# Kernel optimization log

Hardware: AMD Instinct MI355X
Metric: run time of the kernel (lower is better)

The kernel has to match this reference:

```python
import jax, jax.numpy as jnp
import numpy as np
import math

B, T, C, H = 2, 2048, 1024, 16
D = C // H  # head dim = 64

def setup_inputs() -> dict:
    key = jax.random.key(0)
    ks = jax.random.split(key, 9)
    s = 0.02
    return {
        "x": jax.random.normal(ks[0], (B, T, C), dtype=jnp.float32),
        "Wq": jax.random.normal(ks[1], (C, C), dtype=jnp.float32) * s,
        "bq": jax.random.normal(ks[2], (C,), dtype=jnp.float32) * s,
        "Wk": jax.random.normal(ks[3], (C, C), dtype=jnp.float32) * s,
        "bk": jax.random.normal(ks[4], (C,), dtype=jnp.float32) * s,
        "Wv": jax.random.normal(ks[5], (C, C), dtype=jnp.float32) * s,
        "bv": jax.random.normal(ks[6], (C,), dtype=jnp.float32) * s,
        "Wo": jax.random.normal(ks[7], (C, C), dtype=jnp.float32) * s,
        "bo": jax.random.normal(ks[8], (C,), dtype=jnp.float32) * s,
    }

def reference(x, Wq, bq, Wk, bk, Wv, bv, Wo, bo):
    # x: [B, T, C]; torch Linear is y = x @ W.T + b
    Bv_, Tv_, Cv_ = x.shape
    q = (x @ Wq.T + bq).reshape(Bv_, Tv_, H, D)
    k = (x @ Wk.T + bk).reshape(Bv_, Tv_, H, D)
    v = (x @ Wv.T + bv).reshape(Bv_, Tv_, H, D)
    scale = 1.0 / math.sqrt(D)
    # [B, H, Tq, Tk] attention scores
    att = jnp.einsum("bqhd,bkhd->bhqk", q, k) * scale
    causal = jnp.tril(jnp.ones((Tv_, Tv_), dtype=bool))  # [T, T]
    att = jnp.where(causal[None, None, :, :], att, -jnp.inf)
    att = jax.nn.softmax(att, axis=-1)
    y = jnp.einsum("bhqk,bkhd->bqhd", att, v).reshape(Bv_, Tv_, Cv_)
    return y @ Wo.T + bo
```

## Files before the change

kernel.cpp:

```cpp
#include <hip/hip_runtime.h>
#include <hip/hip_bf16.h>
#include <cstdint>
#include <cstddef>

typedef __attribute__((ext_vector_type(8))) short short8;
typedef __attribute__((ext_vector_type(4))) float f32x4;
typedef unsigned int u32;
typedef __attribute__((ext_vector_type(4))) u32 u32x4;

#define MFMA(a,b,c) __builtin_amdgcn_mfma_f32_16x16x32_bf16(a,b,c,0,0,0)

__device__ __forceinline__ void gload_lds16(const void* gptr, void* lptr) {
  __builtin_amdgcn_global_load_lds((const __attribute__((address_space(1))) u32*)gptr,
                                   (__attribute__((address_space(3))) u32*)lptr, 16, 0, 0);
}

template<int N> __device__ __forceinline__ void vm_wait() {
  asm volatile("s_waitcnt vmcnt(%0)" :: "n"(N) : "memory");
}

__device__ __forceinline__ void barrier_sync() {
  asm volatile("" ::: "memory");
  __builtin_amdgcn_s_barrier();
  asm volatile("" ::: "memory");
  __builtin_amdgcn_sched_barrier(0);
}

__device__ __forceinline__ unsigned short f2bf(float f) {
  __hip_bfloat16 h = __float2bfloat16(f);
  return *reinterpret_cast<unsigned short*>(&h);
}

__device__ __forceinline__ short8 ldg8(const unsigned short* p) {
  return *reinterpret_cast<const short8*>(p);
}

__device__ __forceinline__ u32 cvt_pk_bf16(float lo, float hi) {
  u32 r;
  asm("v_cvt_pk_bf16_f32 %0, %1, %2" : "=v"(r) : "v"(lo), "v"(hi));
  return r;
}

__global__ __launch_bounds__(256) void cvt_all_kernel(
    const float* __restrict__ x,
    const float* __restrict__ w0, const float* __restrict__ w1,
    const float* __restrict__ w2, const float* __restrict__ w3,
    unsigned short* __restrict__ xb,
    unsigned short* __restrict__ o0, unsigned short* __restrict__ o1,
    unsigned short* __restrict__ o2, unsigned short* __restrict__ o3)
{
  int id = blockIdx.x * blockDim.x + threadIdx.x;
  const float* in;
  unsigned short* out;
  int idx;
  if (id < 1048576) {
    in = x; out = xb; idx = id;
  } else {
    int r = id - 1048576;
    int z = r >> 18;
    idx = r & 262143;
    in  = (z == 0) ? w0 : (z == 1) ? w1 : (z == 2) ? w2 : w3;
    out = (z == 0) ? o0 : (z == 1) ? o1 : (z == 2) ? o2 : o3;
  }
  float4 f = reinterpret_cast<const float4*>(in)[idx];
  ushort4 o;
  o.x = f2bf(f.x); o.y = f2bf(f.y); o.z = f2bf(f.z); o.w = f2bf(f.w);
  reinterpret_cast<ushort4*>(out)[idx] = o;
}

template<int BM, int BN, int WM, int WN, bool F32OUT>
__device__ __forceinline__ void gemm2_body(
    const unsigned short* __restrict__ A,
    const unsigned short* __restrict__ W,
    const float* __restrict__ bias,
    unsigned short* __restrict__ outb, float* __restrict__ outf,
    int ldo, float oscale, int m0)
{
  constexpr int K = 1024, BK = 32, NT = K / BK;
  constexpr int NTHR = WM * WN * 64;
  constexpr int FM = BM / (WM * 16);
  constexpr int FN = BN / (WN * 16);
  constexpr int NLA = BM * BK * 2 / (NTHR * 16);
  constexpr int NLB = BN * BK * 2 / (NTHR * 16);
  constexpr int NLD = NLA + NLB;

  __shared__ unsigned short As[2][BM * BK];
  __shared__ unsigned short Ws[2][BN * BK];

  const int tid = threadIdx.x;
  const int lane = tid & 63;
  const int wave = tid >> 6;
  const int wm = wave / WN, wn = wave % WN;
  const int wr = wm * FM * 16, wc = wn * FN * 16;
  const int lr = lane >> 4, lc = lane & 15;

  f32x4 acc[FM][FN] = {};

  const char* Ab = (const char*)(A + (size_t)m0 * K);
  const char* Wb = (const char*)W;

#define STAGE(buf, k0)                                                            \
  {                                                                               \
    _Pragma("unroll")                                                             \
    for (int i = 0; i < NLA; ++i) {                                               \
      int L = (i * NTHR + tid) * 16;                                              \
      int row = L >> 6;                                                           \
      int col = L & 63;                                                           \
      gload_lds16(Ab + (size_t)row * 2048 + (k0) * 2 + col, (char*)&As[buf][0] + L); \
    }                                                                             \
    _Pragma("unroll")                                                             \
    for (int i = 0; i < NLB; ++i) {                                               \
      int L = (i * NTHR + tid) * 16;                                              \
      int row = L >> 6;                                                           \
      int col = L & 63;                                                           \
      gload_lds16(Wb + (size_t)row * 2048 + (k0) * 2 + col, (char*)&Ws[buf][0] + L); \
    }                                                                             \
  }

#define COMPUTE(buf)                                                              \
  {                                                                               \
    short8 af[FM], bf[FN];                                                        \
    _Pragma("unroll")                                                             \
    for (int m = 0; m < FM; ++m) {                                                \
      int row = wr + m * 16 + lc;                                                 \
      af[m] = *reinterpret_cast<const short8*>(                                   \
          (const char*)&As[buf][0] + row * 64 + lr * 16);                         \
    }                                                                             \
    _Pragma("unroll")                                                             \
    for (int n = 0; n < FN; ++n) {                                                \
      int row = wc + n * 16 + lc;                                                 \
      bf[n] = *reinterpret_cast<const short8*>(                                   \
          (const char*)&Ws[buf][0] + row * 64 + lr * 16);                         \
    }                                                                             \
    __builtin_amdgcn_s_setprio(1);                                                \
    _Pragma("unroll")                                                             \
    for (int m = 0; m < FM; ++m)                                                  \
      _Pragma("unroll")                                                           \
      for (int n = 0; n < FN; ++n)                                                \
        acc[m][n] = MFMA(af[m], bf[n], acc[m][n]);                                \
    __builtin_amdgcn_s_setprio(0);                                                \
  }

  STAGE(0, 0)
  STAGE(1, BK)
  int cur = 0;
#pragma unroll 1
  for (int kt = 0; kt < NT - 2; ++kt) {
    vm_wait<NLD>();
    barrier_sync();
    COMPUTE(cur)
    barrier_sync();
    STAGE(cur, (kt + 2) * BK)
    cur ^= 1;
  }
  vm_wait<NLD>();
  barrier_sync();
  COMPUTE(cur)
  cur ^= 1;
  vm_wait<0>();
  barrier_sync();
  COMPUTE(cur)

#undef STAGE
#undef COMPUTE

#pragma unroll
  for (int m = 0; m < FM; ++m)
#pragma unroll
    for (int n = 0; n < FN; ++n)
#pragma unroll
      for (int r = 0; r < 4; ++r) {
        int row = m0 + wr + m * 16 + lr * 4 + r;
        int col = wc + n * 16 + lc;
        float v = (acc[m][n][r] + bias[col]) * oscale;
        if (F32OUT) outf[(size_t)row * ldo + col] = v;
        else        outb[(size_t)row * ldo + col] = f2bf(v);
      }
}

__global__ __launch_bounds__(256, 3) void gemm_qkv5(
    const unsigned short* __restrict__ xb,
    const unsigned short* __restrict__ Wqb, const unsigned short* __restrict__ Wkb,
    const unsigned short* __restrict__ Wvb,
    const float* __restrict__ bq, const float* __restrict__ bk, const float* __restrict__ bv,
    unsigned short* __restrict__ Q, unsigned short* __restrict__ Ko, unsigned short* __restrict__ V)
{
  const int i = blockIdx.x;
  const int sw = (i & 7) * 96 + (i >> 3);
  const int z  = sw >> 8;
  const int rr = sw & 255;
  const int m0 = (rr >> 3) * 128;
  const int nr = (rr & 7) * 128;
  const unsigned short* W = ((z == 0) ? Wqb : (z == 1) ? Wkb : Wvb) + (size_t)nr * 1024;
  const float* bias = ((z == 0) ? bq : (z == 1) ? bk : bv) + nr;
  unsigned short* out = ((z == 0) ? Q : (z == 1) ? Ko : V) + nr;
  const float oscale = (z == 0) ? 0.18033688011112042f : 1.0f;
  gemm2_body<128, 128, 2, 2, false>(xb, W, bias, out, nullptr, 1024, oscale, m0);
}

__global__ __launch_bounds__(256, 2) void gemm_out3(
    const unsigned short* __restrict__ Y, const unsigned short* __restrict__ Wob,
    const float* __restrict__ bo, float* __restrict__ out)
{
  const int i = blockIdx.x;
  const int sw = (i & 7) * 64 + (i >> 3);
  const int by = sw >> 3;
  const int bx = sw & 7;
  const int m0 = by * 64;
  const int n0 = bx * 128;
  gemm2_body<64, 128, 2, 2, true>(Y, Wob + (size_t)n0 * 1024, bo + n0, nullptr, out + n0,
                                  1024, 1.0f, m0);
}

__global__ __launch_bounds__(256) void transpose_v(const unsigned short* __restrict__ V,
                                                   unsigned short* __restrict__ VT)
{
  __shared__ unsigned short tile[64 * 68];
  const int tb = blockIdx.x;
  const int bh = blockIdx.y;
  const int b = bh >> 4, h = bh & 15;
  const int tid = threadIdx.x;
  const int t0 = tb * 64;
#pragma unroll
  for (int i = 0; i < 4; ++i) {
    int e = (i * 256 + tid) * 4;
    int t = e >> 6, d = e & 63;
    ushort4 v = *reinterpret_cast<const ushort4*>(&V[((size_t)(b * 2048 + t0 + t)) * 1024 + h * 64 + d]);
    tile[t * 68 + d + 0] = v.x;
    tile[t * 68 + d + 1] = v.y;
    tile[t * 68 + d + 2] = v.z;
    tile[t * 68 + d + 3] = v.w;
  }
  __syncthreads();
#pragma unroll
  for (int i = 0; i < 4; ++i) {
    int e = (i * 256 + tid) * 4;
    int d = e >> 6, tc = e & 63;
    ushort4 w;
    w.x = tile[(tc + 0) * 68 + d];
    w.y = tile[(tc + 1) * 68 + d];
    w.z = tile[(tc + 2) * 68 + d];
    w.w = tile[(tc + 3) * 68 + d];
    *reinterpret_cast<ushort4*>(&VT[((size_t)(bh * 64 + d)) * 2048 + t0 + tc]) = w;
  }
}

__global__ __launch_bounds__(256) void attn_kernel(
    const unsigned short* __restrict__ Q, const unsigned short* __restrict__ K,
    const unsigned short* __restrict__ VT, unsigned short* __restrict__ Y)
{
  __shared__ unsigned short Ks[2][128 * 64];
  __shared__ unsigned short Vs[2][64 * 128];
  __shared__ u32 Pl[4][584];

  const int i   = blockIdx.x;
  const int xcd = i & 7;
  const int j   = i >> 3;
  const int bh  = xcd + 8 * (j & 3);
  const int qb  = 31 - (j >> 2);
  const int b = bh >> 4, h = bh & 15;
  const int tid = threadIdx.x;
  const int wave = tid >> 6;
  const int lane = tid & 63;
  const int lr = lane >> 4;
  const int lc = lane & 15;
  const float M = 4.0f;

  const unsigned short* Kbh = K + (size_t)b * 2048 * 1024 + h * 64;
  const unsigned short* Vbh = VT + (size_t)bh * 64 * 2048;
  u32* pw = Pl[wave];

  u32 ov = 0x3F803F80u;
  u32x4 ones4 = {ov, ov, ov, ov};
  short8 ones = *reinterpret_cast<short8*>(&ones4);

  const int q0 = qb * 64 + wave * 16;
  const unsigned short* qp = &Q[((size_t)(b * 2048 + q0 + lc)) * 1024 + h * 64 + lr * 8];
  short8 qa0 = ldg8(qp);
  short8 qa1 = ldg8(qp + 32);

  f32x4 o[4] = {};
  f32x4 lacc = {};

  const int nt = (qb + 2) >> 1;

#define STAGE_KV(buf, t)                                                          \
  {                                                                               \
    const int tk = (t) * 128;                                                     \
    _Pragma("unroll")                                                             \
    for (int ii = 0; ii < 4; ++ii) {                                              \
      int L = (ii * 256 + tid) * 16;                                              \
      int krow = L >> 7;                                                          \
      int ksrc = (L & 127) ^ ((krow & 7) << 4);                                   \
      gload_lds16((const char*)(Kbh + (size_t)(tk + krow) * 1024) + ksrc,         \
                  (char*)&Ks[buf][0] + L);                                        \
      int vrow = L >> 8;                                                          \
      int vsrc = (L & 255) ^ ((vrow & 15) << 4);                                  \
      gload_lds16((const char*)(Vbh + (size_t)vrow * 2048) + tk * 2 + vsrc,       \
                  (char*)&Vs[buf][0] + L);                                        \
    }                                                                             \
  }

#define COMPUTE_HALF(Kt, Vt, korig, hh)                                           \
  {                                                                               \
    f32x4 s[4] = {};                                                              \
    _Pragma("unroll")                                                             \
    for (int kt = 0; kt < 4; ++kt) {                                              \
      int krow = (hh) * 64 + kt * 16 + lc;                                        \
      int sw = (krow & 7) << 4;                                                   \
      short8 kb0 = *reinterpret_cast<const short8*>((const char*)(Kt) + krow * 128 + ((lr * 16) ^ sw)); \
      short8 kb1 = *reinterpret_cast<const short8*>((const char*)(Kt) + krow * 128 + ((64 + lr * 16) ^ sw)); \
      __builtin_amdgcn_s_setprio(1);                                              \
      s[kt] = MFMA(kb0, qa0, s[kt]);                                              \
      s[kt] = MFMA(kb1, qa1, s[kt]);                                              \
      __builtin_amdgcn_s_setprio(0);                                              \
    }                                                                             \
    float p[4][4];                                                                \
    _Pragma("unroll")                                                             \
    for (int kt = 0; kt < 4; ++kt)                                                \
      _Pragma("unroll")                                                           \
      for (int r = 0; r < 4; ++r)                                                 \
        p[kt][r] = __builtin_amdgcn_exp2f(s[kt][r] - M);                          \
    if ((korig) + 63 > q0) {                                                      \
      _Pragma("unroll")                                                           \
      for (int kt = 0; kt < 4; ++kt)                                              \
        _Pragma("unroll")                                                         \
        for (int r = 0; r < 4; ++r)                                               \
          if ((korig) + kt * 16 + lr * 4 + r > q0 + lc) p[kt][r] = 0.f;           \
    }                                                                             \
    _Pragma("unroll")                                                             \
    for (int kt = 0; kt < 4; ++kt) {                                              \
      uint2 w;                                                                    \
      w.x = cvt_pk_bf16(p[kt][0], p[kt][1]);                                      \
      w.y = cvt_pk_bf16(p[kt][2], p[kt][3]);                                      \
      *reinterpret_cast<uint2*>(&pw[lc * 36 + kt * 8 + lr * 2]) = w;              \
    }                                                                             \
    short8 pa0 = *reinterpret_cast<const short8*>(&pw[lc * 36 + lr * 4]);         \
    short8 pa1 = *reinterpret_cast<const short8*>(&pw[lc * 36 + 16 + lr * 4]);    \
    __builtin_amdgcn_s_setprio(1);                                                \
    lacc = MFMA(pa0, ones, lacc);                                                 \
    lacc = MFMA(pa1, ones, lacc);                                                 \
    __builtin_amdgcn_s_setprio(0);                                                \
    _Pragma("unroll")                                                             \
    for (int ntt = 0; ntt < 4; ++ntt) {                                           \
      int vrow = ntt * 16 + lc;                                                   \
      int vsw = (vrow & 15) << 4;                                                 \
      short8 v0 = *reinterpret_cast<const short8*>((const char*)(Vt) + vrow * 256 + (((hh) * 128 + lr * 16) ^ vsw)); \
      short8 v1 = *reinterpret_cast<const short8*>((const char*)(Vt) + vrow * 256 + (((hh) * 128 + 64 + lr * 16) ^ vsw)); \
      __builtin_amdgcn_s_setprio(1);                                              \
      o[ntt] = MFMA(pa0, v0, o[ntt]);                                             \
      o[ntt] = MFMA(pa1, v1, o[ntt]);                                             \
      __builtin_amdgcn_s_setprio(0);                                              \
    }                                                                             \
  }

  STAGE_KV(0, 0)
  __syncthreads();
  int cur = 0;
#pragma unroll 1
  for (int t = 0; t < nt; ++t) {
    if (t + 1 < nt) STAGE_KV(cur ^ 1, t + 1)

    const int tk0 = t * 128;
    const unsigned short* Kt = Ks[cur];
    const unsigned short* Vt = Vs[cur];

    COMPUTE_HALF(Kt, Vt, tk0, 0)
    if (tk0 + 64 <= q0 + 15) {
      COMPUTE_HALF(Kt, Vt, tk0 + 64, 1)
    }

    __syncthreads();
    cur ^= 1;
  }

#undef STAGE_KV
#undef COMPUTE_HALF

  float rl[4];
#pragma unroll
  for (int r = 0; r < 4; ++r) rl[r] = __builtin_amdgcn_rcpf(lacc[r]);
#pragma unroll
  for (int ntt = 0; ntt < 4; ++ntt)
#pragma unroll
    for (int r = 0; r < 4; ++r) {
      float val = o[ntt][r] * rl[r];
      int row = b * 2048 + q0 + lr * 4 + r;
      Y[(size_t)row * 1024 + h * 64 + ntt * 16 + lc] = f2bf(val);
    }
}

extern "C" void kernel_launch(void* const* d_in, const int* in_sizes, int n_in,
                              void* d_out, int out_size, void* d_ws, size_t ws_size,
                              hipStream_t stream)
{
  const float* x  = (const float*)d_in[0];
  const float* Wq = (const float*)d_in[1];
  const float* bq = (const float*)d_in[2];
  const float* Wk = (const float*)d_in[3];
  const float* bk = (const float*)d_in[4];
  const float* Wv = (const float*)d_in[5];
  const float* bv = (const float*)d_in[6];
  const float* Wo = (const float*)d_in[7];
  const float* bo = (const float*)d_in[8];
  float* out = (float*)d_out;

  char* ws = (char*)d_ws;
  unsigned short* xb  = (unsigned short*)(ws);
  unsigned short* Wqb = (unsigned short*)(ws + 8388608);
  unsigned short* Wkb = (unsigned short*)(ws + 8388608 + 2097152);
  unsigned short* Wvb = (unsigned short*)(ws + 8388608 + 2 * 2097152);
  unsigned short* Wob = (unsigned short*)(ws + 8388608 + 3 * 2097152);
  unsigned short* Qb  = (unsigned short*)(ws + 16777216);
  unsigned short* Kb  = (unsigned short*)(ws + 16777216 + 8388608);
  unsigned short* Vb  = (unsigned short*)(ws + 16777216 + 2 * 8388608);
  unsigned short* VTb = (unsigned short*)(ws + 16777216 + 3 * 8388608);
  unsigned short* Yb  = (unsigned short*)(ws + 16777216 + 4 * 8388608);

  cvt_all_kernel<<<8192, 256, 0, stream>>>(x, Wq, Wk, Wv, Wo, xb, Wqb, Wkb, Wvb, Wob);

  gemm_qkv5<<<768, 256, 0, stream>>>(xb, Wqb, Wkb, Wvb, bq, bk, bv, Qb, Kb, Vb);
  transpose_v<<<dim3(32, 32), 256, 0, stream>>>(Vb, VTb);
  attn_kernel<<<1024, 256, 0, stream>>>(Qb, Kb, VTb, Yb);
  gemm_out3<<<512, 256, 0, stream>>>(Yb, Wob, bo, out);
}
```

Baseline: 105.8 us.

## Split attention key range across waves with register K/V loads and LDS reduction

The attention kernel now has each of the four waves handle all 64 queries of the block and take every fourth 32-key tile. K and V fragments are loaded straight from global memory into registers, with K double-buffered, which drops the shared K/V staging and the per-tile block barriers. The row sum is accumulated in scalar registers instead of with an MFMA against ones. Partial outputs and sums are then reduced across waves through LDS. This removes the inter-wave barriers and LDS staging, but it adds more uncached-style global loads, higher register pressure from 16 accumulators, and a final reduction pass.

Result: slower. 110.5 us (+4.4%).

```diff
diff --git a/kernel.cpp b/kernel.cpp
--- a/kernel.cpp
+++ b/kernel.cpp
@@ -6,7 +6,6 @@
 typedef __attribute__((ext_vector_type(8))) short short8;
 typedef __attribute__((ext_vector_type(4))) float f32x4;
 typedef unsigned int u32;
-typedef __attribute__((ext_vector_type(4))) u32 u32x4;
 
 #define MFMA(a,b,c) __builtin_amdgcn_mfma_f32_16x16x32_bf16(a,b,c,0,0,0)
 
@@ -245,19 +244,16 @@
   }
 }
 
-__global__ __launch_bounds__(256) void attn_kernel(
+__global__ __launch_bounds__(256, 2) void attn_kernel(
     const unsigned short* __restrict__ Q, const unsigned short* __restrict__ K,
     const unsigned short* __restrict__ VT, unsigned short* __restrict__ Y)
 {
-  __shared__ unsigned short Ks[2][128 * 64];
-  __shared__ unsigned short Vs[2][64 * 128];
-  __shared__ u32 Pl[4][584];
+  __shared__ char smem[67584];
 
   const int i   = blockIdx.x;
   const int xcd = i & 7;
-  const int j   = i >> 3;
-  const int bh  = xcd + 8 * (j & 3);
-  const int qb  = 31 - (j >> 2);
+  const int bh  = xcd + 8 * ((i >> 3) & 3);
+  const int qb  = 31 - (i >> 5);
   const int b = bh >> 4, h = bh & 15;
   const int tid = threadIdx.x;
   const int wave = tid >> 6;
@@ -268,126 +264,160 @@
 
   const unsigned short* Kbh = K + (size_t)b * 2048 * 1024 + h * 64;
   const unsigned short* Vbh = VT + (size_t)bh * 64 * 2048;
-  u32* pw = Pl[wave];
-
-  u32 ov = 0x3F803F80u;
-  u32x4 ones4 = {ov, ov, ov, ov};
-  short8 ones = *reinterpret_cast<short8*>(&ones4);
-
-  const int q0 = qb * 64 + wave * 16;
-  const unsigned short* qp = &Q[((size_t)(b * 2048 + q0 + lc)) * 1024 + h * 64 + lr * 8];
-  short8 qa0 = ldg8(qp);
-  short8 qa1 = ldg8(qp + 32);
-
-  f32x4 o[4] = {};
-  f32x4 lacc = {};
-
-  const int nt = (qb + 2) >> 1;
-
-#define STAGE_KV(buf, t)                                                          \
+  char* PlB = smem + wave * 4096;
+
+  const int q0 = qb * 64;
+
+  short8 qf[4][2];
+#pragma unroll
+  for (int qg = 0; qg < 4; ++qg)
+#pragma unroll
+    for (int ds = 0; ds < 2; ++ds)
+      qf[qg][ds] = ldg8(&Q[(size_t)(b * 2048 + q0 + qg * 16 + lc) * 1024 + h * 64 + ds * 32 + lr * 8]);
+
+  f32x4 acc[4][4] = {};
+  float lacc[4] = {};
+
+  const int nt = 2 * qb + 2;
+
+  short8 kfA[2][2], kfB[2][2];
+
+#define LOADK(KF, t_)                                                             \
   {                                                                               \
-    const int tk = (t) * 128;                                                     \
-    _Pragma("unroll")                                                             \
-    for (int ii = 0; ii < 4; ++ii) {                                              \
-      int L = (ii * 256 + tid) * 16;                                              \
-      int krow = L >> 7;                                                          \
-      int ksrc = (L & 127) ^ ((krow & 7) << 4);                                   \
-      gload_lds16((const char*)(Kbh + (size_t)(tk + krow) * 1024) + ksrc,         \
-                  (char*)&Ks[buf][0] + L);                                        \
-      int vrow = L >> 8;                                                          \
-      int vsrc = (L & 255) ^ ((vrow & 15) << 4);                                  \
-      gload_lds16((const char*)(Vbh + (size_t)vrow * 2048) + tk * 2 + vsrc,       \
-                  (char*)&Vs[buf][0] + L);                                        \
-    }                                                                             \
-  }
-
-#define COMPUTE_HALF(Kt, Vt, korig, hh)                                           \
+    const int tkk = (t_) * 32;                                                    \
+    _Pragma("unroll")                                                             \
+    for (int kg = 0; kg < 2; ++kg)                                                \
+      _Pragma("unroll")                                                           \
+      for (int ds = 0; ds < 2; ++ds)                                              \
+        KF[kg][ds] = ldg8(Kbh + (size_t)(tkk + kg * 16 + lc) * 1024 + ds * 32 + lr * 8); \
+  }
+
+#define COMPUTE(KF, t_)                                                           \
   {                                                                               \
-    f32x4 s[4] = {};                                                              \
-    _Pragma("unroll")                                                             \
-    for (int kt = 0; kt < 4; ++kt) {                                              \
-      int krow = (hh) * 64 + kt * 16 + lc;                                        \
-      int sw = (krow & 7) << 4;                                                   \
-      short8 kb0 = *reinterpret_cast<const short8*>((const char*)(Kt) + krow * 128 + ((lr * 16) ^ sw)); \
-      short8 kb1 = *reinterpret_cast<const short8*>((const char*)(Kt) + krow * 128 + ((64 + lr * 16) ^ sw)); \
-      __builtin_amdgcn_s_setprio(1);                                              \
-      s[kt] = MFMA(kb0, qa0, s[kt]);                                              \
-      s[kt] = MFMA(kb1, qa1, s[kt]);                                              \
-      __builtin_amdgcn_s_setprio(0);                                              \
-    }                                                                             \
-    float p[4][4];                                                                \
-    _Pragma("unroll")                                                             \
-    for (int kt = 0; kt < 4; ++kt)                                                \
-      _Pragma("unroll")                                                           \
-      for (int r = 0; r < 4; ++r)                                                 \
-        p[kt][r] = __builtin_amdgcn_exp2f(s[kt][r] - M);                          \
-    if ((korig) + 63 > q0) {                                                      \
-      _Pragma("unroll")                                                           \
-      for (int kt = 0; kt < 4; ++kt)                                              \
+    const int tk0 = (t_) * 32;                                                    \
+    short8 vB[4];                                                                 \
+    _Pragma("unroll")                                                             \
+    for (int dg = 0; dg < 4; ++dg)                                                \
+      vB[dg] = ldg8(Vbh + (size_t)(dg * 16 + lc) * 2048 + tk0 + lr * 8);          \
+    f32x4 sa[2][4] = {};                                                          \
+    __builtin_amdgcn_s_setprio(1);                                                \
+    _Pragma("unroll")                                                             \
+    for (int ds = 0; ds < 2; ++ds)                                                \
+      _Pragma("unroll")                                                           \
+      for (int kg = 0; kg < 2; ++kg)                                              \
+        _Pragma("unroll")                                                         \
+        for (int qg = 0; qg < 4; ++qg)                                            \
+          sa[kg][qg] = MFMA(KF[kg][ds], qf[qg][ds], sa[kg][qg]);                  \
+    __builtin_amdgcn_s_setprio(0);                                                \
+    float p[2][4][4];                                                             \
+    _Pragma("unroll")                                                             \
+    for (int kg = 0; kg < 2; ++kg)                                                \
+      _Pragma("unroll")                                                           \
+      for (int qg = 0; qg < 4; ++qg)                                              \
         _Pragma("unroll")                                                         \
         for (int r = 0; r < 4; ++r)                                               \
-          if ((korig) + kt * 16 + lr * 4 + r > q0 + lc) p[kt][r] = 0.f;           \
+          p[kg][qg][r] = __builtin_amdgcn_exp2f(sa[kg][qg][r] - M);               \
+    if (tk0 + 31 > q0) {                                                          \
+      _Pragma("unroll")                                                           \
+      for (int kg = 0; kg < 2; ++kg)                                              \
+        _Pragma("unroll")                                                         \
+        for (int qg = 0; qg < 4; ++qg)                                            \
+          _Pragma("unroll")                                                       \
+          for (int r = 0; r < 4; ++r)                                             \
+            if (tk0 + kg * 16 + lr * 4 + r > q0 + qg * 16 + lc) p[kg][qg][r] = 0.f; \
     }                                                                             \
     _Pragma("unroll")                                                             \
-    for (int kt = 0; kt < 4; ++kt) {                                              \
-      uint2 w;                                                                    \
-      w.x = cvt_pk_bf16(p[kt][0], p[kt][1]);                                      \
-      w.y = cvt_pk_bf16(p[kt][2], p[kt][3]);                                      \
-      *reinterpret_cast<uint2*>(&pw[lc * 36 + kt * 8 + lr * 2]) = w;              \
-    }                                                                             \
-    short8 pa0 = *reinterpret_cast<const short8*>(&pw[lc * 36 + lr * 4]);         \
-    short8 pa1 = *reinterpret_cast<const short8*>(&pw[lc * 36 + 16 + lr * 4]);    \
+    for (int kg = 0; kg < 2; ++kg)                                                \
+      _Pragma("unroll")                                                           \
+      for (int qg = 0; qg < 4; ++qg)                                              \
+        lacc[qg] += p[kg][qg][0] + p[kg][qg][1] + p[kg][qg][2] + p[kg][qg][3];    \
+    _Pragma("unroll")                                                             \
+    for (int kg = 0; kg < 2; ++kg)                                                \
+      _Pragma("unroll")                                                           \
+      for (int qg = 0; qg < 4; ++qg) {                                            \
+        uint2 w;                                                                  \
+        w.x = cvt_pk_bf16(p[kg][qg][0], p[kg][qg][1]);                            \
+        w.y = cvt_pk_bf16(p[kg][qg][2], p[kg][qg][3]);                            \
+        *reinterpret_cast<uint2*>(PlB + (qg * 16 + lc) * 64 +                     \
+            ((kg * 32 + lr * 8) ^ ((lc & 3) << 4))) = w;                          \
+      }                                                                           \
+    short8 pA[4];                                                                 \
+    _Pragma("unroll")                                                             \
+    for (int qg = 0; qg < 4; ++qg)                                                \
+      pA[qg] = *reinterpret_cast<const short8*>(PlB + (qg * 16 + lc) * 64 +       \
+          ((lr * 16) ^ ((lc & 3) << 4)));                                         \
     __builtin_amdgcn_s_setprio(1);                                                \
-    lacc = MFMA(pa0, ones, lacc);                                                 \
-    lacc = MFMA(pa1, ones, lacc);                                                 \
+    _Pragma("unroll")                                                             \
+    for (int qg = 0; qg < 4; ++qg)                                                \
+      _Pragma("unroll")                                                           \
+      for (int dg = 0; dg < 4; ++dg)                                              \
+        acc[qg][dg] = MFMA(pA[qg], vB[dg], acc[qg][dg]);                          \
     __builtin_amdgcn_s_setprio(0);                                                \
-    _Pragma("unroll")                                                             \
-    for (int ntt = 0; ntt < 4; ++ntt) {                                           \
-      int vrow = ntt * 16 + lc;                                                   \
-      int vsw = (vrow & 15) << 4;                                                 \
-      short8 v0 = *reinterpret_cast<const short8*>((const char*)(Vt) + vrow * 256 + (((hh) * 128 + lr * 16) ^ vsw)); \
-      short8 v1 = *reinterpret_cast<const short8*>((const char*)(Vt) + vrow * 256 + (((hh) * 128 + 64 + lr * 16) ^ vsw)); \
-      __builtin_amdgcn_s_setprio(1);                                              \
-      o[ntt] = MFMA(pa0, v0, o[ntt]);                                             \
-      o[ntt] = MFMA(pa1, v1, o[ntt]);                                             \
-      __builtin_amdgcn_s_setprio(0);                                              \
-    }                                                                             \
-  }
-
-  STAGE_KV(0, 0)
+  }
+
+  int t = wave;
+  if (t < nt) LOADK(kfA, t)
+#pragma unroll 1
+  while (t < nt) {
+    if (t + 4 < nt) LOADK(kfB, t + 4)
+    COMPUTE(kfA, t)
+    t += 4;
+    if (t >= nt) break;
+    if (t + 4 < nt) LOADK(kfA, t + 4)
+    COMPUTE(kfB, t)
+    t += 4;
+  }
+
+#undef LOADK
+#undef COMPUTE
+
+#pragma unroll
+  for (int qg = 0; qg < 4; ++qg) {
+    lacc[qg] += __shfl_xor(lacc[qg], 16);
+    lacc[qg] += __shfl_xor(lacc[qg], 32);
+  }
+
   __syncthreads();
-  int cur = 0;
-#pragma unroll 1
-  for (int t = 0; t < nt; ++t) {
-    if (t + 1 < nt) STAGE_KV(cur ^ 1, t + 1)
-
-    const int tk0 = t * 128;
-    const unsigned short* Kt = Ks[cur];
-    const unsigned short* Vt = Vs[cur];
-
-    COMPUTE_HALF(Kt, Vt, tk0, 0)
-    if (tk0 + 64 <= q0 + 15) {
-      COMPUTE_HALF(Kt, Vt, tk0 + 64, 1)
+  float* Ored = (float*)smem;
+#pragma unroll
+  for (int qg = 0; qg < 4; ++qg) {
+#pragma unroll
+    for (int dg = 0; dg < 4; ++dg)
+#pragma unroll
+      for (int r = 0; r < 4; ++r)
+        Ored[(size_t)(wave * 64 + qg * 16 + lr * 4 + r) * 66 + dg * 16 + lc] = acc[qg][dg][r];
+    if (lr == 0)
+      Ored[(size_t)(wave * 64 + qg * 16 + lc) * 66 + 64] = lacc[qg];
+  }
+  __syncthreads();
+
+  {
+    const int qoff = lane & 15;
+    const int dblk = lane >> 4;
+    const int qrow = wave * 16 + qoff;
+    float s[16];
+#pragma unroll
+    for (int j = 0; j < 16; ++j) s[j] = 0.f;
+    float lsum = 0.f;
+#pragma unroll
+    for (int pz = 0; pz < 4; ++pz) {
+      const float* rp = &Ored[(size_t)(pz * 64 + qrow) * 66];
+#pragma unroll
+      for (int j = 0; j < 16; ++j) s[j] += rp[dblk * 16 + j];
+      lsum += rp[64];
     }
-
-    __syncthreads();
-    cur ^= 1;
-  }
-
-#undef STAGE_KV
-#undef COMPUTE_HALF
-
-  float rl[4];
-#pragma unroll
-  for (int r = 0; r < 4; ++r) rl[r] = __builtin_amdgcn_rcpf(lacc[r]);
-#pragma unroll
-  for (int ntt = 0; ntt < 4; ++ntt)
-#pragma unroll
-    for (int r = 0; r < 4; ++r) {
-      float val = o[ntt][r] * rl[r];
-      int row = b * 2048 + q0 + lr * 4 + r;
-      Y[(size_t)row * 1024 + h * 64 + ntt * 16 + lc] = f2bf(val);
+    float rl = __builtin_amdgcn_rcpf(lsum);
+    unsigned short* yp = &Y[(size_t)(b * 2048 + q0 + qrow) * 1024 + h * 64 + dblk * 16];
+#pragma unroll
+    for (int j = 0; j < 16; j += 4) {
+      ushort4 w;
+      w.x = f2bf(s[j + 0] * rl);
+      w.y = f2bf(s[j + 1] * rl);
+      w.z = f2bf(s[j + 2] * rl);
+      w.w = f2bf(s[j + 3] * rl);
+      *reinterpret_cast<ushort4*>(yp + j) = w;
     }
+  }
 }
 
 extern "C" void kernel_launch(void* const* d_in, const int* in_sizes, int n_in,
```
